# Performance work log

Hardware: AMD Instinct MI355X
Metric: run time of the kernel (lower is better)

Reference implementation:

```python
import jax, jax.numpy as jnp
import numpy as np

B, T, D, H = 4, 2048, 1024, 16
HD = D // H  # head_dim = 64

def setup_inputs() -> dict:
    key = jax.random.key(0)
    k1, k2, k3 = jax.random.split(key, 3)
    x = jax.random.normal(k1, (B, T, D), dtype=jnp.float32)
    Wqkv = jax.random.normal(k2, (D, 3 * D), dtype=jnp.float32) * (D ** -0.5)
    Wout = jax.random.normal(k3, (D, D), dtype=jnp.float32) * (D ** -0.5)
    return {"x": x, "Wqkv": Wqkv, "Wout": Wout}

def reference(x, Wqkv, Wout):
    Bb, Tt, C = x.shape
    qkv = x @ Wqkv  # [B,T,3D]
    qkv = qkv.reshape(Bb, Tt, 3, H, HD)
    q, k, v = qkv[:, :, 0], qkv[:, :, 1], qkv[:, :, 2]  # each [B,T,H,HD]
    scale = 1.0 / np.sqrt(HD)
    # scores [B,H,T,T]
    attn = jnp.einsum('bqhd,bkhd->bhqk', q, k) * scale
    causal = jnp.tril(jnp.ones((Tt, Tt), dtype=bool))
    attn = jnp.where(causal[None, None], attn, -jnp.inf)
    attn = jax.nn.softmax(attn, axis=-1)
    out = jnp.einsum('bhqk,bkhd->bqhd', attn, v).reshape(Bb, Tt, C)
    return out @ Wout
```

## Files before the change

### kernel.cpp

```cpp
#include <hip/hip_runtime.h>
#include <hip/hip_bf16.h>

#define T_SEQ 2048
#define NBATCH 4
#define NHEAD 16
#define HDIM 64
#define DMODEL 1024

typedef __bf16 bf16x8 __attribute__((ext_vector_type(8)));
typedef float f32x4 __attribute__((ext_vector_type(4)));
typedef float f32x16 __attribute__((ext_vector_type(16)));

__device__ __forceinline__ unsigned short f2bf(float f) {
  unsigned int u = __builtin_bit_cast(unsigned int, f);
  u += 0x7fffu + ((u >> 16) & 1u);
  return (unsigned short)(u >> 16);
}

__device__ __forceinline__ float fexp2(float x) {
  float r;
  asm("v_exp_f32 %0, %1" : "=v"(r) : "v"(x));
  return r;
}

__device__ __forceinline__ void async_cp16(void* lds, const void* g) {
  __builtin_amdgcn_global_load_lds((const __attribute__((address_space(1))) void*)g,
                                   (__attribute__((address_space(3))) void*)lds,
                                   16, 0, 0);
}

__global__ __launch_bounds__(256) void prep_k(const float* __restrict__ x,
                                              const float* __restrict__ Wqkv,
                                              const float* __restrict__ Wout,
                                              unsigned short* __restrict__ xb,
                                              unsigned short* __restrict__ wqkvT,
                                              unsigned short* __restrict__ woutT) {
  __shared__ float tile[32][33];
  const int bidx = blockIdx.x;
  const int t = threadIdx.x;
  if (bidx < 8192) {
    int i = (bidx * 256 + t) * 4;
    float4 v = *(const float4*)(x + i);
    ushort4 o;
    o.x = f2bf(v.x); o.y = f2bf(v.y); o.z = f2bf(v.z); o.w = f2bf(v.w);
    *(ushort4*)(xb + i) = o;
    return;
  }
  const float* in;
  unsigned short* out;
  int R, C, c0, r0;
  if (bidx < 8192 + 3072) {
    int tb = bidx - 8192;
    in = Wqkv; out = wqkvT; R = 1024; C = 3072;
    c0 = (tb % 96) * 32; r0 = (tb / 96) * 32;
  } else {
    int tb = bidx - 11264;
    in = Wout; out = woutT; R = 1024; C = 1024;
    c0 = (tb & 31) * 32; r0 = (tb >> 5) * 32;
  }
  const int tx = t & 31, ty = t >> 5;
#pragma unroll
  for (int j = 0; j < 32; j += 8)
    tile[ty + j][tx] = in[(size_t)(r0 + ty + j) * C + c0 + tx];
  __syncthreads();
#pragma unroll
  for (int j = 0; j < 32; j += 8)
    out[(size_t)(c0 + ty + j) * R + r0 + tx] = f2bf(tile[tx][ty + j]);
}

__global__ __launch_bounds__(512, 4) void gemm1_v5_k(const unsigned short* __restrict__ A,
                                                     const unsigned short* __restrict__ Bt,
                                                     unsigned short* __restrict__ Qb,
                                                     unsigned short* __restrict__ Kb,
                                                     unsigned short* __restrict__ Vt) {
  __shared__ uint4 ldsv[5120];
  char* lds = (char*)ldsv;
  const int t = threadIdx.x;
  const int w = t >> 6, lane = t & 63;
  const int lr = lane & 15, lg = lane >> 4;
  const int wr = w >> 2, wc = w & 3;
  const int bid = blockIdx.x;
  const int wid = (bid & 7) * 128 + (bid >> 3);
  const int m0 = (wid >> 4) * 128, n0 = (wid & 15) * 192;

  const int row0 = t >> 3;
  const int colc0 = (t & 7) ^ (row0 & 7);
  const int stU = w * 1024;

  const unsigned short* Abase = A + (size_t)(m0 + row0) * 1024 + colc0 * 8;
  const unsigned short* Bbase = Bt + (size_t)(n0 + row0) * 1024 + colc0 * 8;

#define STGA(pb, h, kt)                                                          \
  async_cp16(lds + (pb) + (h) * 8192 + stU,                                      \
             Abase + (size_t)(h) * 64 * 1024 + (kt) * 64)
#define STGB(pb, s, kt)                                                          \
  async_cp16(lds + (pb) + 16384 + (s) * 8192 + stU,                              \
             Bbase + (size_t)(s) * 64 * 1024 + (kt) * 64)
#define VM3() asm volatile("s_waitcnt vmcnt(3)" ::: "memory")
#define BAR()                                                                    \
  {                                                                              \
    __builtin_amdgcn_s_barrier();                                                \
    __builtin_amdgcn_sched_barrier(0);                                           \
  }

  f32x4 acc[4][3];
#pragma unroll
  for (int mi = 0; mi < 4; ++mi)
#pragma unroll
    for (int ni = 0; ni < 3; ++ni) acc[mi][ni] = (f32x4){0.f, 0.f, 0.f, 0.f};

  STGA(0, 0, 0); STGA(0, 1, 0);
  STGB(0, 0, 0); STGB(0, 1, 0); STGB(0, 2, 0);
  STGB(40960, 0, 1); STGB(40960, 1, 1); STGB(40960, 2, 1);
  VM3();
  BAR();

  bf16x8 bfr[3][2], af[2][2];

#define LDB(pb)                                                                      \
  {                                                                                  \
    _Pragma("unroll") for (int ni = 0; ni < 3; ++ni) _Pragma("unroll")               \
        for (int kk = 0; kk < 2; ++kk) {                                             \
      int rrow = wc * 48 + ni * 16 + lr;                                             \
      int cc = (kk * 4 + lg) ^ (lr & 7);                                             \
      bfr[ni][kk] = *(const bf16x8*)(lds + (pb) + 16384 + rrow * 128 + cc * 16);     \
    }                                                                                \
  }
#define LDA(Q, pb, S)                                                                \
  {                                                                                  \
    _Pragma("unroll") for (int kk = 0; kk < 2; ++kk) {                               \
      int rrow = wr * 64 + (Q) * 16 + lr;                                            \
      int cc = (kk * 4 + lg) ^ (lr & 7);                                             \
      af[S][kk] = *(const bf16x8*)(lds + (pb) + rrow * 128 + cc * 16);               \
    }                                                                                \
  }
#define MM(Q, S)                                                                     \
  {                                                                                  \
    __builtin_amdgcn_s_setprio(1);                                                   \
    _Pragma("unroll") for (int kk = 0; kk < 2; ++kk) _Pragma("unroll")               \
        for (int ni = 0; ni < 3; ++ni) acc[Q][ni] =                                  \
            __builtin_amdgcn_mfma_f32_16x16x32_bf16(af[S][kk], bfr[ni][kk],          \
                                                    acc[Q][ni], 0, 0, 0);            \
    __builtin_amdgcn_s_setprio(0);                                                   \
  }

  const int P0 = 0, P1 = 40960;
  for (int I = 0; I < 8; ++I) {
    const int t1 = 2 * I + 1;
    const int t2 = (2 * I + 2 < 16) ? 2 * I + 2 : 15;
    const int t3 = (2 * I + 3 < 16) ? 2 * I + 3 : 15;
    LDB(P0); LDA(0, P0, 0); LDA(1, P0, 1);
    STGA(P1, 0, t1); STGA(P1, 1, t1);
    BAR(); MM(0, 0); MM(1, 1); BAR();
    LDA(2, P0, 0); LDA(3, P0, 1);
    STGB(P0, 0, t2); STGB(P0, 1, t2); STGB(P0, 2, t2);
    BAR(); MM(2, 0); MM(3, 1); VM3(); BAR();
    LDB(P1); LDA(0, P1, 0); LDA(1, P1, 1);
    STGA(P0, 0, t2); STGA(P0, 1, t2);
    BAR(); MM(0, 0); MM(1, 1); BAR();
    LDA(2, P1, 0); LDA(3, P1, 1);
    STGB(P1, 0, t3); STGB(P1, 1, t3); STGB(P1, 2, t3);
    BAR(); MM(2, 0); MM(3, 1); VM3(); BAR();
  }

#pragma unroll
  for (int mi = 0; mi < 4; ++mi) {
#pragma unroll
    for (int ni = 0; ni < 3; ++ni) {
      int gm = m0 + wr * 64 + mi * 16 + lg * 4;
      int gn = n0 + wc * 48 + ni * 16 + lr;
      f32x4 v = acc[mi][ni];
      int b = gm >> 11, tt = gm & 2047;
      int sel = gn >> 10, rem = gn & 1023;
      int h = rem >> 6, hd = rem & 63;
      int bh = b * NHEAD + h;
      if (sel == 0) {
        unsigned short* p = Qb + ((size_t)bh * T_SEQ + tt) * HDIM + hd;
#pragma unroll
        for (int r = 0; r < 4; ++r)
          p[(size_t)r * HDIM] = f2bf(v[r] * (0.125f * 1.44269504f));
      } else if (sel == 1) {
        unsigned short* p = Kb + (size_t)bh * T_SEQ * HDIM + (tt >> 5) * 2048 +
                            (hd >> 4) * 512 + ((hd >> 3) & 1) * 256 + (tt & 31) * 8 +
                            (hd & 7);
#pragma unroll
        for (int r = 0; r < 4; ++r) p[r * 8] = f2bf(v[r]);
      } else {
        unsigned short* p = Vt + (size_t)bh * T_SEQ * HDIM + (tt >> 4) * 1024 +
                            ((tt >> 3) & 1) * 512 + (hd >> 5) * 256 + (hd & 31) * 8 +
                            (tt & 7);
        ushort4 o;
        o.x = f2bf(v[0]); o.y = f2bf(v[1]); o.z = f2bf(v[2]); o.w = f2bf(v[3]);
        *(ushort4*)p = o;
      }
    }
  }
#undef STGA
#undef STGB
#undef VM3
#undef BAR
#undef LDB
#undef LDA
#undef MM
}

template <int EPI, int NT>
__global__ __launch_bounds__(512, 1) void gemm_8ph2_k(const unsigned short* __restrict__ A,
                                                      const unsigned short* __restrict__ Bt,
                                                      unsigned short* __restrict__ Qb,
                                                      unsigned short* __restrict__ Kb,
                                                      unsigned short* __restrict__ Vt,
                                                      float* __restrict__ Cout) {
  __shared__ uint4 ldsv[6144];
  char* lds = (char*)ldsv;
  const int t = threadIdx.x;
  const int w = t >> 6, lane = t & 63;
  const int lr = lane & 15, lg = lane >> 4;
  const int wr = w >> 1, wc = w & 1;
  const int bid = blockIdx.x;
  const int perx = (NT * 32) / 8;
  const int wid = (bid & 7) * perx + (bid >> 3);
  const int m0 = (wid / NT) * 256, n0 = (wid % NT) * 128;

  const int row0 = t >> 3;
  const int colc0 = (t & 7) ^ (row0 & 7);
  const int stU = w * 1024;

  const unsigned short* Abase = A + (size_t)(m0 + row0) * 1024 + colc0 * 8;
  const unsigned short* Bbase = Bt + (size_t)(n0 + row0) * 1024 + colc0 * 8;

#define STGA(dst, h, kt)                                                        \
  {                                                                             \
    const unsigned short* _s = Abase + (size_t)(h) * 128 * 1024 + (kt) * 64;    \
    async_cp16(lds + (dst) + (h) * 16384 + stU, _s);                            \
    async_cp16(lds + (dst) + (h) * 16384 + stU + 8192, _s + 64 * 1024);         \
  }
#define STGB(dst, kt)                                                           \
  {                                                                             \
    const unsigned short* _s = Bbase + (kt) * 64;                               \
    async_cp16(lds + (dst) + 32768 + stU, _s);                                  \
    async_cp16(lds + (dst) + 32768 + stU + 8192, _s + 64 * 1024);               \
  }
#define VM2() asm volatile("s_waitcnt vmcnt(2)" ::: "memory")
#define BAR()                                                                   \
  {                                                                             \
    __builtin_amdgcn_s_barrier();                                               \
    __builtin_amdgcn_sched_barrier(0);                                          \
  }

  f32x4 acc[4][4];
#pragma unroll
  for (int mi = 0; mi < 4; ++mi)
#pragma unroll
    for (int ni = 0; ni < 4; ++ni) acc[mi][ni] = (f32x4){0.f, 0.f, 0.f, 0.f};

  STGA(0, 0, 0);
  STGA(0, 1, 0);
  STGB(0, 0);
  STGB(49152, 1);
  VM2();
  BAR();

  bf16x8 bfr[4][2], af[2][2];
  const int ldsAh = (wr >> 1) * 16384;
  const int arow0 = (wr & 1) * 64;
  const int brow0 = wc * 64;

#define LDB(pbase)                                                                   \
  {                                                                                  \
    _Pragma("unroll") for (int ni = 0; ni < 4; ++ni) _Pragma("unroll")               \
        for (int kk = 0; kk < 2; ++kk) {                                             \
      int rrow = brow0 + ni * 16 + lr;                                               \
      int cc = (kk * 4 + lg) ^ (lr & 7);                                             \
      bfr[ni][kk] = *(const bf16x8*)(lds + (pbase) + 32768 + rrow * 128 + cc * 16);  \
    }                                                                                \
  }
#define LDA(Q, pbase)                                                                \
  {                                                                                  \
    _Pragma("unroll") for (int m2 = 0; m2 < 2; ++m2) _Pragma("unroll")               \
        for (int kk = 0; kk < 2; ++kk) {                                             \
      int rrow = arow0 + (2 * (Q) + m2) * 16 + lr;                                   \
      int cc = (kk * 4 + lg) ^ (lr & 7);                                             \
      af[m2][kk] = *(const bf16x8*)(lds + (pbase) + ldsAh + rrow * 128 + cc * 16);   \
    }                                                                                \
  }
#define MM(Q)                                                                        \
  {                                                                                  \
    __builtin_amdgcn_s_setprio(1);                                                   \
    _Pragma("unroll") for (int m2 = 0; m2 < 2; ++m2) _Pragma("unroll")               \
        for (int kk = 0; kk < 2; ++kk) _Pragma("unroll") for (int ni = 0; ni < 4;    \
                                                              ++ni) acc[2 * (Q) +    \
                                                                        m2][ni] =    \
            __builtin_amdgcn_mfma_f32_16x16x32_bf16(af[m2][kk], bfr[ni][kk],         \
                                                    acc[2 * (Q) + m2][ni], 0, 0, 0); \
    __builtin_amdgcn_s_setprio(0);                                                   \
  }

  for (int I = 0; I < 8; ++I) {
    const int t1o = 2 * I + 1;
    const int t2e = (2 * I + 2 < 16) ? 2 * I + 2 : 15;
    const int t3o = (2 * I + 3 < 16) ? 2 * I + 3 : 15;
    LDB(0); LDA(0, 0); STGA(49152, 0, t1o); BAR(); MM(0); BAR();
    LDA(1, 0); STGA(49152, 1, t1o); STGB(0, t2e); BAR(); MM(1); VM2(); BAR();
    LDB(49152); LDA(0, 49152); STGA(0, 0, t2e); BAR(); MM(0); BAR();
    LDA(1, 49152); STGA(0, 1, t2e); STGB(49152, t3o); BAR(); MM(1); VM2(); BAR();
  }

#pragma unroll
  for (int mi = 0; mi < 4; ++mi) {
#pragma unroll
    for (int ni = 0; ni < 4; ++ni) {
      int gm = m0 + wr * 64 + mi * 16 + lg * 4;
      int gn = n0 + wc * 64 + ni * 16 + lr;
      f32x4 v = acc[mi][ni];
#pragma unroll
      for (int r = 0; r < 4; ++r) Cout[(size_t)(gm + r) * (NT * 128) + gn] = v[r];
    }
  }
#undef STGA
#undef STGB
#undef VM2
#undef BAR
#undef LDB
#undef LDA
#undef MM
}

#define PVJJ(Sv, B, JJ, Oa, Obb)                                                              \
  {                                                                                           \
    unsigned w0, w1, w2, w3;                                                                  \
    asm("v_cvt_pk_bf16_f32 %0, %1, %2" : "=v"(w0) : "v"(Sv[B + 0]), "v"(Sv[B + 1]));          \
    asm("v_cvt_pk_bf16_f32 %0, %1, %2" : "=v"(w1) : "v"(Sv[B + 2]), "v"(Sv[B + 3]));          \
    asm("v_cvt_pk_bf16_f32 %0, %1, %2" : "=v"(w2) : "v"(Sv[B + 4]), "v"(Sv[B + 5]));          \
    asm("v_cvt_pk_bf16_f32 %0, %1, %2" : "=v"(w3) : "v"(Sv[B + 6]), "v"(Sv[B + 7]));          \
    asm("v_permlane32_swap_b32 %0, %1" : "+v"(w0), "+v"(w2));                                 \
    asm("v_permlane32_swap_b32 %0, %1" : "+v"(w1), "+v"(w3));                                 \
    union { unsigned u[4]; bf16x8 v; } pf;                                                    \
    pf.u[0] = w0; pf.u[1] = w1; pf.u[2] = w2; pf.u[3] = w3;                                   \
    bf16x8 vfa = *(const bf16x8*)(bv + (JJ) * 2048 + hi * 1024 + lq * 16);                    \
    bf16x8 vfb = *(const bf16x8*)(bv + (JJ) * 2048 + hi * 1024 + lq * 16 + 512);              \
    __builtin_amdgcn_s_setprio(1);                                                            \
    Oa = __builtin_amdgcn_mfma_f32_32x32x16_bf16(vfa, pf.v, Oa, 0, 0, 0);                     \
    Obb = __builtin_amdgcn_mfma_f32_32x32x16_bf16(vfb, pf.v, Obb, 0, 0, 0);                   \
    __builtin_amdgcn_s_setprio(0);                                                            \
  }

__global__ __launch_bounds__(256, 4) void attn_fwd11_k(const unsigned short* __restrict__ Qb,
                                                       const unsigned short* __restrict__ Kb,
                                                       const unsigned short* __restrict__ Vt,
                                                       unsigned short* __restrict__ Ob) {
  __shared__ char lds[32768];
  const int tid = threadIdx.x;
  const int w = tid >> 6, lane = tid & 63;
  const int lq = lane & 31, hi = lane >> 5;
  const int bid = blockIdx.x;
  const int xcd = bid & 7, i = bid >> 3;
  const int bh = xcd * 8 + (i & 7);
  const int s = 15 - (i >> 3);
  const int qb = s * 4 + w;
  const int qw = qb * 32;
  const int P = 2 * (s + 1);

  const unsigned short* Qp = Qb + (size_t)bh * T_SEQ * HDIM;
  const char* Ksrc = (const char*)(Kb + (size_t)bh * T_SEQ * HDIM);
  const char* Vsrc = (const char*)(Vt + (size_t)bh * T_SEQ * HDIM);
  const int b = bh >> 4, h = bh & 15;

#define ASTG(bb, p)                                                                   \
  {                                                                                   \
    async_cp16(lds + (bb) * 16384 + w * 1024, Ksrc + (size_t)(p) * 8192 + tid * 16);  \
    async_cp16(lds + (bb) * 16384 + 4096 + w * 1024,                                  \
               Ksrc + (size_t)(p) * 8192 + 4096 + tid * 16);                          \
    async_cp16(lds + (bb) * 16384 + 8192 + w * 1024,                                  \
               Vsrc + (size_t)(p) * 8192 + tid * 16);                                 \
    async_cp16(lds + (bb) * 16384 + 12288 + w * 1024,                                 \
               Vsrc + (size_t)(p) * 8192 + 4096 + tid * 16);                          \
  }

  bf16x8 qf[4];
#pragma unroll
  for (int dj = 0; dj < 4; ++dj)
    qf[dj] = *(const bf16x8*)(Qp + (size_t)(qw + lq) * HDIM + dj * 16 + hi * 8);

  f32x16 O0, O1;
#pragma unroll
  for (int r = 0; r < 16; ++r) { O0[r] = 0.f; O1[r] = 0.f; }
  float m_run = -30000.0f, l_run = 0.f;

  auto smax_pair = [&](f32x16& S0, f32x16& S1) {
    float m8[8];
#pragma unroll
    for (int r = 0; r < 8; ++r)
      m8[r] = fmaxf(fmaxf(S0[r], S0[r + 8]), fmaxf(S1[r], S1[r + 8]));
#pragma unroll
    for (int r = 0; r < 4; ++r) m8[r] = fmaxf(m8[r], m8[r + 4]);
    float pmax = fmaxf(fmaxf(m8[0], m8[1]), fmaxf(m8[2], m8[3]));
    pmax = fmaxf(pmax, __shfl_xor(pmax, 32, 64));
    if (__any(pmax > m_run + 11.5f)) {
      float mn = fmaxf(m_run, pmax);
      float al = fexp2(m_run - mn);
      m_run = mn;
      l_run *= al;
#pragma unroll
      for (int r = 0; r < 16; ++r) { O0[r] *= al; O1[r] *= al; }
    }
#pragma unroll
    for (int r = 0; r < 16; ++r) {
      S0[r] = fexp2(S0[r] - m_run);
      S1[r] = fexp2(S1[r] - m_run);
    }
    float s8[8];
#pragma unroll
    for (int r = 0; r < 8; ++r) s8[r] = (S0[r] + S0[r + 8]) + (S1[r] + S1[r + 8]);
#pragma unroll
    for (int r = 0; r < 4; ++r) s8[r] += s8[r + 4];
    float ps = (s8[0] + s8[1]) + (s8[2] + s8[3]);
    ps += __shfl_xor(ps, 32, 64);
    l_run += ps;
  };

  auto smax_single = [&](f32x16& S0) {
    float m8[8];
#pragma unroll
    for (int r = 0; r < 8; ++r) m8[r] = fmaxf(S0[r], S0[r + 8]);
#pragma unroll
    for (int r = 0; r < 4; ++r) m8[r] = fmaxf(m8[r], m8[r + 4]);
    float pmax = fmaxf(fmaxf(m8[0], m8[1]), fmaxf(m8[2], m8[3]));
    pmax = fmaxf(pmax, __shfl_xor(pmax, 32, 64));
    if (__any(pmax > m_run + 11.5f)) {
      float mn = fmaxf(m_run, pmax);
      float al = fexp2(m_run - mn);
      m_run = mn;
      l_run *= al;
#pragma unroll
      for (int r = 0; r < 16; ++r) { O0[r] *= al; O1[r] *= al; }
    }
#pragma unroll
    for (int r = 0; r < 16; ++r) S0[r] = fexp2(S0[r] - m_run);
    float s8[8];
#pragma unroll
    for (int r = 0; r < 8; ++r) s8[r] = S0[r] + S0[r + 8];
#pragma unroll
    for (int r = 0; r < 4; ++r) s8[r] += s8[r + 4];
    float ps = (s8[0] + s8[1]) + (s8[2] + s8[3]);
    ps += __shfl_xor(ps, 32, 64);
    l_run += ps;
  };

  ASTG(0, 0);
  __syncthreads();

  for (int p = 0; p < P; ++p) {
    if (p + 1 < P) ASTG((p + 1) & 1, p + 1);
    const char* bk = lds + (p & 1) * 16384;
    const char* bv = bk + 8192;
    const int t0 = 2 * p, t1 = 2 * p + 1;
    if (t0 <= qb) {
      const bool v1 = (t1 <= qb);
      f32x16 S0, S1;
#pragma unroll
      for (int r = 0; r < 16; ++r) { S0[r] = 0.f; S1[r] = 0.f; }
      __builtin_amdgcn_s_setprio(1);
#pragma unroll
      for (int dj = 0; dj < 4; ++dj) {
        bf16x8 k0 = *(const bf16x8*)(bk + dj * 1024 + lane * 16);
        S0 = __builtin_amdgcn_mfma_f32_32x32x16_bf16(k0, qf[dj], S0, 0, 0, 0);
      }
      if (v1) {
#pragma unroll
        for (int dj = 0; dj < 4; ++dj) {
          bf16x8 k1 = *(const bf16x8*)(bk + 4096 + dj * 1024 + lane * 16);
          S1 = __builtin_amdgcn_mfma_f32_32x32x16_bf16(k1, qf[dj], S1, 0, 0, 0);
        }
      }
      __builtin_amdgcn_s_setprio(0);
      if (t0 == qb) {
#pragma unroll
        for (int r = 0; r < 16; ++r) {
          int kvl = (r & 3) + 8 * (r >> 2) + 4 * hi;
          S0[r] = (kvl > lq) ? -30000.0f : S0[r];
        }
      }
      if (v1 && t1 == qb) {
#pragma unroll
        for (int r = 0; r < 16; ++r) {
          int kvl = (r & 3) + 8 * (r >> 2) + 4 * hi;
          S1[r] = (kvl > lq) ? -30000.0f : S1[r];
        }
      }
      if (v1) {
        smax_pair(S0, S1);
        PVJJ(S0, 0, 0, O0, O1); PVJJ(S0, 8, 1, O0, O1);
        PVJJ(S1, 0, 2, O0, O1); PVJJ(S1, 8, 3, O0, O1);
      } else {
        smax_single(S0);
        PVJJ(S0, 0, 0, O0, O1); PVJJ(S0, 8, 1, O0, O1);
      }
    }
    __syncthreads();
  }

  const float linv = 1.0f / l_run;
  unsigned short* op = Ob + ((size_t)(b * T_SEQ + qw + lq)) * DMODEL + h * HDIM;
#pragma unroll
  for (int g = 0; g < 4; ++g) {
    ushort4 o;
    o.x = f2bf(O0[4 * g + 0] * linv);
    o.y = f2bf(O0[4 * g + 1] * linv);
    o.z = f2bf(O0[4 * g + 2] * linv);
    o.w = f2bf(O0[4 * g + 3] * linv);
    *(ushort4*)(op + 8 * g + 4 * hi) = o;
    ushort4 o2;
    o2.x = f2bf(O1[4 * g + 0] * linv);
    o2.y = f2bf(O1[4 * g + 1] * linv);
    o2.z = f2bf(O1[4 * g + 2] * linv);
    o2.w = f2bf(O1[4 * g + 3] * linv);
    *(ushort4*)(op + 32 + 8 * g + 4 * hi) = o2;
  }
#undef ASTG
}

extern "C" void kernel_launch(void* const* d_in, const int* in_sizes, int n_in,
                              void* d_out, int out_size, void* d_ws, size_t ws_size,
                              hipStream_t stream) {
  const float* x = (const float*)d_in[0];
  const float* Wqkv = (const float*)d_in[1];
  const float* Wout = (const float*)d_in[2];
  float* out = (float*)d_out;

  unsigned short* ws = (unsigned short*)d_ws;
  const size_t nx = (size_t)NBATCH * T_SEQ * DMODEL;
  unsigned short* xb    = ws;
  unsigned short* wqkvT = xb + nx;
  unsigned short* woutT = wqkvT + (size_t)3 * DMODEL * DMODEL;
  unsigned short* Qb    = woutT + (size_t)DMODEL * DMODEL;
  unsigned short* Kb    = Qb + nx;
  unsigned short* Vt    = Kb + nx;
  unsigned short* Ab    = Vt + nx;
  size_t need = 2ull * (5 * nx + 4ull * DMODEL * DMODEL);
  if (ws_size < need) return;

  prep_k<<<dim3(12288), dim3(256), 0, stream>>>(x, Wqkv, Wout, xb, wqkvT, woutT);
  gemm1_v5_k<<<dim3(1024), dim3(512), 0, stream>>>(xb, wqkvT, Qb, Kb, Vt);
  attn_fwd11_k<<<dim3(1024), dim3(256), 0, stream>>>(Qb, Kb, Vt, Ab);
  gemm_8ph2_k<1, 8><<<dim3(256), dim3(512), 0, stream>>>(Ab, woutT, nullptr, nullptr,
                                                         nullptr, out);
}
```

Measured before the change: 142.6 us.

## Retile output projection GEMM to 128x128 blocks with more resident blocks per CU

Replaces the 256x128-tile output-projection GEMM (256 blocks, one block per CU) with a 128x128-tile version launched as 512 blocks. Warps are rearranged 2x4, LDS use drops to 64KB, and launch bounds allow several blocks per CU. The aim is to fill all 256 CUs with more than one block each and improve latency hiding and tail balance. The cost is less operand reuse per tile, which means more global and LDS traffic per FLOP.

Measured after the change: 139.1 us (median of 2 runs). -2.4%, faster.

```diff
diff --git a/kernel.cpp b/kernel.cpp
--- a/kernel.cpp
+++ b/kernel.cpp
@@ -204,23 +204,18 @@
 #undef MM
 }
 
-template <int EPI, int NT>
-__global__ __launch_bounds__(512, 1) void gemm_8ph2_k(const unsigned short* __restrict__ A,
-                                                      const unsigned short* __restrict__ Bt,
-                                                      unsigned short* __restrict__ Qb,
-                                                      unsigned short* __restrict__ Kb,
-                                                      unsigned short* __restrict__ Vt,
-                                                      float* __restrict__ Cout) {
-  __shared__ uint4 ldsv[6144];
+__global__ __launch_bounds__(512, 4) void gemm2_v5_k(const unsigned short* __restrict__ A,
+                                                     const unsigned short* __restrict__ Bt,
+                                                     float* __restrict__ Cout) {
+  __shared__ uint4 ldsv[4096];
   char* lds = (char*)ldsv;
   const int t = threadIdx.x;
   const int w = t >> 6, lane = t & 63;
   const int lr = lane & 15, lg = lane >> 4;
-  const int wr = w >> 1, wc = w & 1;
+  const int wr = w >> 2, wc = w & 3;
   const int bid = blockIdx.x;
-  const int perx = (NT * 32) / 8;
-  const int wid = (bid & 7) * perx + (bid >> 3);
-  const int m0 = (wid / NT) * 256, n0 = (wid % NT) * 128;
+  const int wid = (bid & 7) * 64 + (bid >> 3);
+  const int m0 = (wid >> 3) * 128, n0 = (wid & 7) * 128;
 
   const int row0 = t >> 3;
   const int colc0 = (t & 7) ^ (row0 & 7);
@@ -229,92 +224,88 @@
   const unsigned short* Abase = A + (size_t)(m0 + row0) * 1024 + colc0 * 8;
   const unsigned short* Bbase = Bt + (size_t)(n0 + row0) * 1024 + colc0 * 8;
 
-#define STGA(dst, h, kt)                                                        \
-  {                                                                             \
-    const unsigned short* _s = Abase + (size_t)(h) * 128 * 1024 + (kt) * 64;    \
-    async_cp16(lds + (dst) + (h) * 16384 + stU, _s);                            \
-    async_cp16(lds + (dst) + (h) * 16384 + stU + 8192, _s + 64 * 1024);         \
-  }
-#define STGB(dst, kt)                                                           \
-  {                                                                             \
-    const unsigned short* _s = Bbase + (kt) * 64;                               \
-    async_cp16(lds + (dst) + 32768 + stU, _s);                                  \
-    async_cp16(lds + (dst) + 32768 + stU + 8192, _s + 64 * 1024);               \
-  }
+#define STGA(pb, h, kt)                                                          \
+  async_cp16(lds + (pb) + (h) * 8192 + stU,                                      \
+             Abase + (size_t)(h) * 64 * 1024 + (kt) * 64)
+#define STGB(pb, s, kt)                                                          \
+  async_cp16(lds + (pb) + 16384 + (s) * 8192 + stU,                              \
+             Bbase + (size_t)(s) * 64 * 1024 + (kt) * 64)
 #define VM2() asm volatile("s_waitcnt vmcnt(2)" ::: "memory")
-#define BAR()                                                                   \
-  {                                                                             \
-    __builtin_amdgcn_s_barrier();                                               \
-    __builtin_amdgcn_sched_barrier(0);                                          \
-  }
-
-  f32x4 acc[4][4];
+#define BAR()                                                                    \
+  {                                                                              \
+    __builtin_amdgcn_s_barrier();                                                \
+    __builtin_amdgcn_sched_barrier(0);                                           \
+  }
+
+  f32x4 acc[4][2];
 #pragma unroll
   for (int mi = 0; mi < 4; ++mi)
 #pragma unroll
-    for (int ni = 0; ni < 4; ++ni) acc[mi][ni] = (f32x4){0.f, 0.f, 0.f, 0.f};
-
-  STGA(0, 0, 0);
-  STGA(0, 1, 0);
-  STGB(0, 0);
-  STGB(49152, 1);
+    for (int ni = 0; ni < 2; ++ni) acc[mi][ni] = (f32x4){0.f, 0.f, 0.f, 0.f};
+
+  STGA(0, 0, 0); STGA(0, 1, 0);
+  STGB(0, 0, 0); STGB(0, 1, 0);
+  STGB(32768, 0, 1); STGB(32768, 1, 1);
   VM2();
   BAR();
 
-  bf16x8 bfr[4][2], af[2][2];
-  const int ldsAh = (wr >> 1) * 16384;
-  const int arow0 = (wr & 1) * 64;
-  const int brow0 = wc * 64;
-
-#define LDB(pbase)                                                                   \
+  bf16x8 bfr[2][2], af[2][2];
+
+#define LDB(pb)                                                                      \
   {                                                                                  \
-    _Pragma("unroll") for (int ni = 0; ni < 4; ++ni) _Pragma("unroll")               \
+    _Pragma("unroll") for (int ni = 0; ni < 2; ++ni) _Pragma("unroll")               \
         for (int kk = 0; kk < 2; ++kk) {                                             \
-      int rrow = brow0 + ni * 16 + lr;                                               \
+      int rrow = wc * 32 + ni * 16 + lr;                                             \
       int cc = (kk * 4 + lg) ^ (lr & 7);                                             \
-      bfr[ni][kk] = *(const bf16x8*)(lds + (pbase) + 32768 + rrow * 128 + cc * 16);  \
+      bfr[ni][kk] = *(const bf16x8*)(lds + (pb) + 16384 + rrow * 128 + cc * 16);     \
     }                                                                                \
   }
-#define LDA(Q, pbase)                                                                \
+#define LDA(Q, pb, S)                                                                \
   {                                                                                  \
-    _Pragma("unroll") for (int m2 = 0; m2 < 2; ++m2) _Pragma("unroll")               \
-        for (int kk = 0; kk < 2; ++kk) {                                             \
-      int rrow = arow0 + (2 * (Q) + m2) * 16 + lr;                                   \
+    _Pragma("unroll") for (int kk = 0; kk < 2; ++kk) {                               \
+      int rrow = wr * 64 + (Q) * 16 + lr;                                            \
       int cc = (kk * 4 + lg) ^ (lr & 7);                                             \
-      af[m2][kk] = *(const bf16x8*)(lds + (pbase) + ldsAh + rrow * 128 + cc * 16);   \
+      af[S][kk] = *(const bf16x8*)(lds + (pb) + rrow * 128 + cc * 16);               \
     }                                                                                \
   }
-#define MM(Q)                                                                        \
+#define MM(Q, S)                                                                     \
   {                                                                                  \
     __builtin_amdgcn_s_setprio(1);                                                   \
-    _Pragma("unroll") for (int m2 = 0; m2 < 2; ++m2) _Pragma("unroll")               \
-        for (int kk = 0; kk < 2; ++kk) _Pragma("unroll") for (int ni = 0; ni < 4;    \
-                                                              ++ni) acc[2 * (Q) +    \
-                                                                        m2][ni] =    \
-            __builtin_amdgcn_mfma_f32_16x16x32_bf16(af[m2][kk], bfr[ni][kk],         \
-                                                    acc[2 * (Q) + m2][ni], 0, 0, 0); \
+    _Pragma("unroll") for (int kk = 0; kk < 2; ++kk) _Pragma("unroll")               \
+        for (int ni = 0; ni < 2; ++ni) acc[Q][ni] =                                  \
+            __builtin_amdgcn_mfma_f32_16x16x32_bf16(af[S][kk], bfr[ni][kk],          \
+                                                    acc[Q][ni], 0, 0, 0);            \
     __builtin_amdgcn_s_setprio(0);                                                   \
   }
 
+  const int P0 = 0, P1 = 32768;
   for (int I = 0; I < 8; ++I) {
-    const int t1o = 2 * I + 1;
-    const int t2e = (2 * I + 2 < 16) ? 2 * I + 2 : 15;
-    const int t3o = (2 * I + 3 < 16) ? 2 * I + 3 : 15;
-    LDB(0); LDA(0, 0); STGA(49152, 0, t1o); BAR(); MM(0); BAR();
-    LDA(1, 0); STGA(49152, 1, t1o); STGB(0, t2e); BAR(); MM(1); VM2(); BAR();
-    LDB(49152); LDA(0, 49152); STGA(0, 0, t2e); BAR(); MM(0); BAR();
-    LDA(1, 49152); STGA(0, 1, t2e); STGB(49152, t3o); BAR(); MM(1); VM2(); BAR();
+    const int t1 = 2 * I + 1;
+    const int t2 = (2 * I + 2 < 16) ? 2 * I + 2 : 15;
+    const int t3 = (2 * I + 3 < 16) ? 2 * I + 3 : 15;
+    LDB(P0); LDA(0, P0, 0); LDA(1, P0, 1);
+    STGA(P1, 0, t1); STGA(P1, 1, t1);
+    BAR(); MM(0, 0); MM(1, 1); BAR();
+    LDA(2, P0, 0); LDA(3, P0, 1);
+    STGB(P0, 0, t2); STGB(P0, 1, t2);
+    BAR(); MM(2, 0); MM(3, 1); VM2(); BAR();
+    LDB(P1); LDA(0, P1, 0); LDA(1, P1, 1);
+    STGA(P0, 0, t2); STGA(P0, 1, t2);
+    BAR(); MM(0, 0); MM(1, 1); BAR();
+    LDA(2, P1, 0); LDA(3, P1, 1);
+    STGB(P1, 0, t3); STGB(P1, 1, t3);
+    BAR(); MM(2, 0); MM(3, 1); VM2(); BAR();
   }
 
 #pragma unroll
   for (int mi = 0; mi < 4; ++mi) {
 #pragma unroll
-    for (int ni = 0; ni < 4; ++ni) {
+    for (int ni = 0; ni < 2; ++ni) {
       int gm = m0 + wr * 64 + mi * 16 + lg * 4;
-      int gn = n0 + wc * 64 + ni * 16 + lr;
+      int gn = n0 + wc * 32 + ni * 16 + lr;
       f32x4 v = acc[mi][ni];
 #pragma unroll
-      for (int r = 0; r < 4; ++r) Cout[(size_t)(gm + r) * (NT * 128) + gn] = v[r];
+      for (int r = 0; r < 4; ++r) Cout[(size_t)(gm + r) * DMODEL + gn] = v[r];
     }
   }
 #undef STGA
@@ -543,6 +534,5 @@
   prep_k<<<dim3(12288), dim3(256), 0, stream>>>(x, Wqkv, Wout, xb, wqkvT, woutT);
   gemm1_v5_k<<<dim3(1024), dim3(512), 0, stream>>>(xb, wqkvT, Qb, Kb, Vt);
   attn_fwd11_k<<<dim3(1024), dim3(256), 0, stream>>>(Qb, Kb, Vt, Ab);
-  gemm_8ph2_k<1, 8><<<dim3(256), dim3(512), 0, stream>>>(Ab, woutT, nullptr, nullptr,
-                                                         nullptr, out);
-}
+  gemm2_v5_k<<<dim3(512), dim3(512), 0, stream>>>(Ab, woutT, out);
+}
```
